# Performance work log

Hardware: AMD Instinct MI355X
Metric: run time of the kernel (lower is better)

Reference implementation:

```python
import jax, jax.numpy as jnp
import numpy as np

TIME = 4096
DIM = 2048
DT_TAU = 0.1 / 1.0  # dt / tau


def setup_inputs() -> dict:
    key = jax.random.key(0)
    k1, k2, k3, k4 = jax.random.split(key, 4)
    inputs = jax.random.normal(k1, (TIME, 1, DIM), dtype=jnp.float32)
    W = jax.random.normal(k2, (DIM, DIM), dtype=jnp.float32) * 0.02  # recurrent weight (nn.Linear, bias=False)
    bias = jax.random.normal(k3, (1, DIM), dtype=jnp.float32)
    initial = jax.random.normal(k4, (1, DIM), dtype=jnp.float32)
    return {"inputs": inputs, "W": W, "bias": bias, "initial": initial}


def reference(inputs, W, bias, initial):
    # states[0] = initial; states[t+1] = s*(1-dt/tau) + (dt/tau)*(sigmoid(s+bias)@W.T + inputs[t])
    def step(state, x_t):
        f = jax.nn.sigmoid(state + bias) @ W.T  # [1, dim]
        new_state = state * (1.0 - DT_TAU) + DT_TAU * (f + x_t)
        return new_state, new_state

    _, rest = jax.lax.scan(step, initial, inputs[: TIME - 1])  # rest: [time-1, 1, dim]
    return jnp.concatenate([initial[None], rest], axis=0)  # [time, 1, dim]
```

## Files before the change

### kernel.cpp

```cpp
#include <hip/hip_runtime.h>
#include <hip/hip_fp16.h>
#include <stdint.h>

#define TIME_STEPS 4096
#define DIM        2048
#define NWG        256
#define NTH        128
#define NWAVE      512
#define RPW        4

typedef uint32_t u32x4 __attribute__((ext_vector_type(4)));
typedef _Float16 h2f16 __attribute__((ext_vector_type(2)));


__device__ __forceinline__ uint32_t umin32(uint32_t a, uint32_t b) { return a < b ? a : b; }

__device__ __forceinline__ float dot2f(uint32_t packed, h2f16 w, float acc) {
#if __has_builtin(__builtin_amdgcn_fdot2)
  return __builtin_amdgcn_fdot2(__builtin_bit_cast(h2f16, packed), w, acc, false);
#else
  h2f16 a = __builtin_bit_cast(h2f16, packed);
  acc = fmaf((float)a.x, (float)w.x, acc);
  return fmaf((float)a.y, (float)w.y, acc);
#endif
}

template<int NSLOT>
__global__ __launch_bounds__(NTH, 1) void ctrnn_kernel(
    const float* __restrict__ x,
    const float* __restrict__ W,
    const float* __restrict__ bias,
    const float* __restrict__ initial,
    float* __restrict__ out,
    uint32_t* __restrict__ actbuf,
    uint32_t* __restrict__ progress)
{
  const int lane = threadIdx.x & 63;
  const int wid  = (blockIdx.x << 1) | (threadIdx.x >> 6);
  const int s    = lane >> 2;
  const int rr   = lane & 3;
  const int row0 = wid * RPW;
  const int cb   = s * 128 + rr * 4;

  h2f16 w2[4][16];
  #pragma unroll
  for (int m = 0; m < 4; ++m) {
    const float* wr = W + (size_t)(row0 + m) * DIM + cb;
    #pragma unroll
    for (int k = 0; k < 8; ++k) {
      w2[m][2*k]   = h2f16{(_Float16)wr[k*16 + 0], (_Float16)wr[k*16 + 1]};
      w2[m][2*k+1] = h2f16{(_Float16)wr[k*16 + 2], (_Float16)wr[k*16 + 3]};
    }
  }

  float v = 0.f, bj = 0.f, xv = 0.f;
  if (lane < RPW) {
    const int j = row0 + lane;
    v  = initial[j];
    bj = bias[j];
    xv = x[j];
    out[j] = v;
    const float a0 = 1.0f / (1.0f + __expf(-(v + bj)));
    __half h = __float2half_rn(a0);
    uint16_t hb; __builtin_memcpy(&hb, &h, 2);
    __hip_atomic_store(&actbuf[j], (1u << 16) | hb,
                       __ATOMIC_RELAXED, __HIP_MEMORY_SCOPE_AGENT);
  }

  uint32_t prog_seen = 0;

  for (int t = 0; t < TIME_STEPS - 1; ++t) {
    float xn = 0.f;
    if (lane < RPW) xn = x[(size_t)(t + 1) * DIM + row0 + lane];

    const uint32_t needtag = (uint32_t)(t + 1);
    const uint32_t thresh  = needtag << 16;
    const uint32_t* src = actbuf + (size_t)(t & (NSLOT - 1)) * DIM + cb;

    u32x4 q[8];
    for (;;) {
      asm volatile(
        "global_load_dwordx4 %0, %8, off sc1\n\t"
        "global_load_dwordx4 %1, %8, off offset:64 sc1\n\t"
        "global_load_dwordx4 %2, %8, off offset:128 sc1\n\t"
        "global_load_dwordx4 %3, %8, off offset:192 sc1\n\t"
        "global_load_dwordx4 %4, %8, off offset:256 sc1\n\t"
        "global_load_dwordx4 %5, %8, off offset:320 sc1\n\t"
        "global_load_dwordx4 %6, %8, off offset:384 sc1\n\t"
        "global_load_dwordx4 %7, %8, off offset:448 sc1\n\t"
        "s_waitcnt vmcnt(0)"
        : "=&v"(q[0]), "=&v"(q[1]), "=&v"(q[2]), "=&v"(q[3]),
          "=&v"(q[4]), "=&v"(q[5]), "=&v"(q[6]), "=&v"(q[7])
        : "v"(src)
        : "memory");
      __builtin_amdgcn_sched_barrier(0);

      uint32_t mn = 0xFFFFFFFFu;
      #pragma unroll
      for (int k = 0; k < 8; ++k)
        mn = umin32(mn, umin32(umin32(q[k][0], q[k][1]),
                               umin32(q[k][2], q[k][3])));
      if (__all((int)(mn >= thresh))) break;
    }

    if (lane == 0)
      __hip_atomic_store(&progress[wid], needtag,
                         __ATOMIC_RELAXED, __HIP_MEMORY_SCOPE_AGENT);

    float a0 = 0.f, a1 = 0.f, a2 = 0.f, a3 = 0.f;
    #pragma unroll
    for (int k = 0; k < 8; ++k) {
      const uint32_t lo = __builtin_amdgcn_perm(q[k][1], q[k][0], 0x05040100u);
      const uint32_t hi = __builtin_amdgcn_perm(q[k][3], q[k][2], 0x05040100u);
      a0 = dot2f(lo, w2[0][2*k], a0); a0 = dot2f(hi, w2[0][2*k+1], a0);
      a1 = dot2f(lo, w2[1][2*k], a1); a1 = dot2f(hi, w2[1][2*k+1], a1);
      a2 = dot2f(lo, w2[2][2*k], a2); a2 = dot2f(hi, w2[2][2*k+1], a2);
      a3 = dot2f(lo, w2[3][2*k], a3); a3 = dot2f(hi, w2[3][2*k+1], a3);
    }

    const float t0 = a0 + __shfl_xor(a0, 1, 64);
    const float t1 = a1 + __shfl_xor(a1, 1, 64);
    const float t2 = a2 + __shfl_xor(a2, 1, 64);
    const float t3 = a3 + __shfl_xor(a3, 1, 64);
    const float m01 = (lane & 1) ? t1 : t0;
    const float m23 = (lane & 1) ? t3 : t2;
    const float u01 = m01 + __shfl_xor(m01, 2, 64);
    const float u23 = m23 + __shfl_xor(m23, 2, 64);
    float p = (lane & 2) ? u23 : u01;
    p += __shfl_xor(p, 4, 64);
    p += __shfl_xor(p, 8, 64);
    p += __shfl_xor(p, 16, 64);
    p += __shfl_xor(p, 32, 64);

    if (t >= NSLOT - 1) {
      const uint32_t need = (uint32_t)(t + 2 - NSLOT);
      if (need > prog_seen) {
        for (;;) {
          uint32_t mn = 0xFFFFFFFFu;
          #pragma unroll
          for (int i = 0; i < 8; ++i)
            mn = umin32(mn, __hip_atomic_load(&progress[lane + 64*i],
                              __ATOMIC_RELAXED, __HIP_MEMORY_SCOPE_AGENT));
          uint32_t qq;
          qq = (uint32_t)__shfl_xor((int)mn, 1, 64);  mn = umin32(mn, qq);
          qq = (uint32_t)__shfl_xor((int)mn, 2, 64);  mn = umin32(mn, qq);
          qq = (uint32_t)__shfl_xor((int)mn, 4, 64);  mn = umin32(mn, qq);
          qq = (uint32_t)__shfl_xor((int)mn, 8, 64);  mn = umin32(mn, qq);
          qq = (uint32_t)__shfl_xor((int)mn, 16, 64); mn = umin32(mn, qq);
          qq = (uint32_t)__shfl_xor((int)mn, 32, 64); mn = umin32(mn, qq);
          if (mn >= need) { prog_seen = mn; break; }
        }
      }
    }

    if (lane < RPW) {
      v  = 0.9f * v + 0.1f * (p + xv);
      xv = xn;
      out[(size_t)(t + 1) * DIM + row0 + lane] = v;
      const float a = 1.0f / (1.0f + __expf(-(v + bj)));
      __half h = __float2half_rn(a);
      uint16_t hb; __builtin_memcpy(&hb, &h, 2);
      const uint32_t e = ((uint32_t)(t + 2) << 16) | hb;
      __hip_atomic_store(&actbuf[(size_t)((t + 1) & (NSLOT - 1)) * DIM + row0 + lane], e,
                         __ATOMIC_RELAXED, __HIP_MEMORY_SCOPE_AGENT);
    }
  }
}

extern "C" void kernel_launch(void* const* d_in, const int* in_sizes, int n_in,
                              void* d_out, int out_size, void* d_ws, size_t ws_size,
                              hipStream_t stream) {
  const float* x       = (const float*)d_in[0];
  const float* W       = (const float*)d_in[1];
  const float* bias    = (const float*)d_in[2];
  const float* initial = (const float*)d_in[3];
  float* out           = (float*)d_out;

  uint32_t* actbuf = (uint32_t*)d_ws;

  const size_t need32 = (size_t)32 * DIM * 4 + NWAVE * 4;
  void* kfun;
  size_t actbytes;
  if (ws_size >= need32) { kfun = (void*)ctrnn_kernel<32>; actbytes = (size_t)32 * DIM * 4; }
  else                   { kfun = (void*)ctrnn_kernel<8>;  actbytes = (size_t)8  * DIM * 4; }

  uint32_t* progress = (uint32_t*)((char*)d_ws + actbytes);

  hipMemsetAsync(d_ws, 0, actbytes + NWAVE * 4, stream);

  void* args[] = { (void*)&x, (void*)&W, (void*)&bias, (void*)&initial,
                   (void*)&out, (void*)&actbuf, (void*)&progress };
  hipLaunchCooperativeKernel(kfun, dim3(NWG), dim3(NTH), args, 0, stream);
}
```

Measured before the change: 9.834 ms.

## Replicate activation ring buffer per block group and prefetch inputs two steps ahead

Measured after the change: 12.36 ms. 1.26x slower.

```diff
diff --git a/kernel.cpp b/kernel.cpp
--- a/kernel.cpp
+++ b/kernel.cpp
@@ -25,7 +25,7 @@
 #endif
 }
 
-template<int NSLOT>
+template<int NSLOT, int NCOPY>
 __global__ __launch_bounds__(NTH, 1) void ctrnn_kernel(
     const float* __restrict__ x,
     const float* __restrict__ W,
@@ -42,6 +42,8 @@
   const int row0 = wid * RPW;
   const int cb   = s * 128 + rr * 4;
 
+  uint32_t* mybuf = actbuf + (size_t)(blockIdx.x & (NCOPY - 1)) * NSLOT * DIM;
+
   h2f16 w2[4][16];
   #pragma unroll
   for (int m = 0; m < 4; ++m) {
@@ -53,29 +55,30 @@
     }
   }
 
-  float v = 0.f, bj = 0.f, xv = 0.f;
+  float v = 0.f, bj = 0.f, xv = 0.f, xw = 0.f;
   if (lane < RPW) {
     const int j = row0 + lane;
     v  = initial[j];
     bj = bias[j];
     xv = x[j];
+    xw = x[DIM + j];
     out[j] = v;
     const float a0 = 1.0f / (1.0f + __expf(-(v + bj)));
     __half h = __float2half_rn(a0);
     uint16_t hb; __builtin_memcpy(&hb, &h, 2);
-    __hip_atomic_store(&actbuf[j], (1u << 16) | hb,
-                       __ATOMIC_RELAXED, __HIP_MEMORY_SCOPE_AGENT);
+    const uint32_t e = (1u << 16) | hb;
+    #pragma unroll
+    for (int c = 0; c < NCOPY; ++c)
+      __hip_atomic_store(&actbuf[(size_t)c * NSLOT * DIM + j], e,
+                         __ATOMIC_RELAXED, __HIP_MEMORY_SCOPE_AGENT);
   }
 
   uint32_t prog_seen = 0;
 
   for (int t = 0; t < TIME_STEPS - 1; ++t) {
-    float xn = 0.f;
-    if (lane < RPW) xn = x[(size_t)(t + 1) * DIM + row0 + lane];
-
     const uint32_t needtag = (uint32_t)(t + 1);
     const uint32_t thresh  = needtag << 16;
-    const uint32_t* src = actbuf + (size_t)(t & (NSLOT - 1)) * DIM + cb;
+    const uint32_t* src = mybuf + (size_t)(t & (NSLOT - 1)) * DIM + cb;
 
     u32x4 q[8];
     for (;;) {
@@ -102,6 +105,9 @@
                                umin32(q[k][2], q[k][3])));
       if (__all((int)(mn >= thresh))) break;
     }
+
+    float xn = 0.f;
+    if (lane < RPW && t + 2 < TIME_STEPS) xn = x[(size_t)(t + 2) * DIM + row0 + lane];
 
     if (lane == 0)
       __hip_atomic_store(&progress[wid], needtag,
@@ -155,14 +161,18 @@
 
     if (lane < RPW) {
       v  = 0.9f * v + 0.1f * (p + xv);
-      xv = xn;
+      xv = xw;
+      xw = xn;
       out[(size_t)(t + 1) * DIM + row0 + lane] = v;
       const float a = 1.0f / (1.0f + __expf(-(v + bj)));
       __half h = __float2half_rn(a);
       uint16_t hb; __builtin_memcpy(&hb, &h, 2);
       const uint32_t e = ((uint32_t)(t + 2) << 16) | hb;
-      __hip_atomic_store(&actbuf[(size_t)((t + 1) & (NSLOT - 1)) * DIM + row0 + lane], e,
-                         __ATOMIC_RELAXED, __HIP_MEMORY_SCOPE_AGENT);
+      const size_t slotoff = (size_t)((t + 1) & (NSLOT - 1)) * DIM + row0 + lane;
+      #pragma unroll
+      for (int c = 0; c < NCOPY; ++c)
+        __hip_atomic_store(&actbuf[(size_t)c * NSLOT * DIM + slotoff], e,
+                           __ATOMIC_RELAXED, __HIP_MEMORY_SCOPE_AGENT);
     }
   }
 }
@@ -178,11 +188,15 @@
 
   uint32_t* actbuf = (uint32_t*)d_ws;
 
-  const size_t need32 = (size_t)32 * DIM * 4 + NWAVE * 4;
+  const size_t ring8 = (size_t)8 * 16 * DIM * 4;
+  const size_t ring2 = (size_t)2 * 16 * DIM * 4;
+  const size_t ring1 = (size_t)1 *  8 * DIM * 4;
+
   void* kfun;
   size_t actbytes;
-  if (ws_size >= need32) { kfun = (void*)ctrnn_kernel<32>; actbytes = (size_t)32 * DIM * 4; }
-  else                   { kfun = (void*)ctrnn_kernel<8>;  actbytes = (size_t)8  * DIM * 4; }
+  if (ws_size >= ring8 + NWAVE * 4)      { kfun = (void*)ctrnn_kernel<16, 8>; actbytes = ring8; }
+  else if (ws_size >= ring2 + NWAVE * 4) { kfun = (void*)ctrnn_kernel<16, 2>; actbytes = ring2; }
+  else                                   { kfun = (void*)ctrnn_kernel<8, 1>;  actbytes = ring1; }
 
   uint32_t* progress = (uint32_t*)((char*)d_ws + actbytes);
 
```
